# Performance work log

Hardware: AMD Instinct MI355X
Metric: run time of the kernel (lower is better)

The kernel has to match this reference:

```python
import jax, jax.numpy as jnp
import numpy as np

EPS = 1e-5

def rmsnorm(x, w):
    var = jnp.mean(x * x, axis=-1, keepdims=True)
    return x * jax.lax.rsqrt(var + EPS) * w

def apply_rope(x, cos, sin):
    # x: [B, S, H, D], cos/sin: [S, D//2]; llama-style complex rotation over pairs
    B, S, H, D = x.shape
    xr = x.reshape(B, S, H, D // 2, 2)
    x0, x1 = xr[..., 0], xr[..., 1]
    c = cos[None, :, None, :]
    s = sin[None, :, None, :]
    o0 = x0 * c - x1 * s
    o1 = x0 * s + x1 * c
    return jnp.stack([o0, o1], axis=-1).reshape(B, S, H, D)

def setup_inputs() -> dict:
    key = jax.random.key(0)
    ks = jax.random.split(key, 8)
    B, S, dim = 2, 2048, 2048
    H, nope, rope = 16, 128, 64
    q_lr, kv_lr = 1536, 512
    hd = nope + rope
    x = jax.random.normal(ks[0], (B, S, dim), jnp.float32)
    wd_q = jax.random.normal(ks[1], (dim, q_lr), jnp.float32) * (dim ** -0.5)
    wu_q = jax.random.normal(ks[2], (q_lr, H * hd), jnp.float32) * (q_lr ** -0.5)
    q_norm_w = jnp.ones((q_lr,), jnp.float32)
    wd_kv = jax.random.normal(ks[3], (dim, kv_lr + rope), jnp.float32) * (dim ** -0.5)
    wu_kv = jax.random.normal(ks[4], (kv_lr, H * 2 * nope), jnp.float32) * (kv_lr ** -0.5)
    kv_norm_w = jnp.ones((kv_lr,), jnp.float32)
    wo = jax.random.normal(ks[5], (H * nope, dim), jnp.float32) * ((H * nope) ** -0.5)
    pos = jnp.arange(S, dtype=jnp.float32)
    inv_freq = 1.0 / (10000.0 ** (jnp.arange(0, rope, 2, dtype=jnp.float32) / rope))
    ang = pos[:, None] * inv_freq[None, :]  # [S, rope//2]
    return {"x": x, "wd_q": wd_q, "wu_q": wu_q, "q_norm_w": q_norm_w,
            "wd_kv": wd_kv, "wu_kv": wu_kv, "kv_norm_w": kv_norm_w, "wo": wo,
            "cos": jnp.cos(ang), "sin": jnp.sin(ang), "start_pos": 0}

def reference(x, wd_q, wu_q, q_norm_w, wd_kv, wu_kv, kv_norm_w, wo, cos, sin, start_pos):
    B, S, dim = x.shape
    H, nope, rope = 16, 128, 64
    kv_lr = 512
    hd = nope + rope
    # low-rank Q projection + RMSNorm
    cq = x @ wd_q
    xq = rmsnorm(cq, q_norm_w) @ wu_q
    xq = xq.reshape(B, S, H, hd)
    xq_nope, xq_rope = xq[..., :nope], xq[..., nope:]
    # low-rank KV projection
    kvd = x @ wd_kv
    ckv, xk_rope = kvd[..., :kv_lr], kvd[..., kv_lr:]
    xk_rope = xk_rope.reshape(B, S, 1, rope)
    kvu = (rmsnorm(ckv, kv_norm_w) @ wu_kv).reshape(B, S, H, 2 * nope)
    xk_nope, xv = kvu[..., :nope], kvu[..., nope:]
    # partial RoPE
    xq_rope = apply_rope(xq_rope, cos, sin)
    xk_rope = apply_rope(xk_rope, cos, sin)
    xk_rope = jnp.broadcast_to(xk_rope, (B, S, H, rope))
    q = jnp.concatenate([xq_nope, xq_rope], axis=-1)  # [B,S,H,192]
    k = jnp.concatenate([xk_nope, xk_rope], axis=-1)
    # causal SDPA
    scale = 1.0 / jnp.sqrt(jnp.float32(hd))
    scores = jnp.einsum('bqhd,bkhd->bhqk', q, k) * scale
    mask = jnp.tril(jnp.ones((S, S), bool))
    scores = jnp.where(mask[None, None], scores, jnp.finfo(scores.dtype).min)
    attn = jax.nn.softmax(scores, axis=-1)
    out = jnp.einsum('bhqk,bkhd->bqhd', attn, xv).reshape(B, S, H * nope)
    return out @ wo
```

## Files before the change

### kernel.cpp

```cpp
#include <hip/hip_runtime.h>
#include <hip/hip_bf16.h>

#define S_LEN 2048
#define NHEAD 16
#define NOPE 128
#define ROPE 64
#define HD 192

typedef unsigned short ushort_t;
typedef __attribute__((ext_vector_type(8))) short short8;
typedef __attribute__((ext_vector_type(4))) float f32x4;

#define AS1 __attribute__((address_space(1)))
#define AS3 __attribute__((address_space(3)))

__device__ __forceinline__ unsigned short f2bf(float f) {
  unsigned int u = __float_as_uint(f);
  return (unsigned short)((u + 0x7FFFu + ((u >> 16) & 1u)) >> 16);
}

__global__ __launch_bounds__(256) void prep_k(const float* __restrict__ x, ushort_t* __restrict__ xb,
                                              const float* __restrict__ wd_q, ushort_t* __restrict__ wdqt,
                                              const float* __restrict__ wd_kv, ushort_t* __restrict__ wdkvt,
                                              const float* __restrict__ wu_q, ushort_t* __restrict__ wuqt,
                                              const float* __restrict__ wu_kv, ushort_t* __restrict__ wukvt,
                                              const float* __restrict__ wo, ushort_t* __restrict__ wot) {
  int id = blockIdx.x;
  if (id < 4096) {
    const int i = id * 256 + threadIdx.x;
    const float4 v0 = *(const float4*)&x[(size_t)i * 8];
    const float4 v1 = *(const float4*)&x[(size_t)i * 8 + 4];
    union { uint4 u; ushort_t s[8]; } pk;
    pk.s[0] = f2bf(v0.x); pk.s[1] = f2bf(v0.y); pk.s[2] = f2bf(v0.z); pk.s[3] = f2bf(v0.w);
    pk.s[4] = f2bf(v1.x); pk.s[5] = f2bf(v1.y); pk.s[6] = f2bf(v1.z); pk.s[7] = f2bf(v1.w);
    *(uint4*)&xb[(size_t)i * 8] = pk.u;
    return;
  }
  id -= 4096;
  const float* B; ushort_t* Bt; int K, N, gx;
  if (id < 3072)               { B = wd_q;  Bt = wdqt;  K = 2048; N = 1536; gx = 48;  }
  else if ((id -= 3072) < 1280){ B = wd_kv; Bt = wdkvt; K = 2048; N = 576;  gx = 20;  }
  else if ((id -= 1280) < 4608){ B = wu_q;  Bt = wuqt;  K = 1536; N = 3072; gx = 96;  }
  else if ((id -= 4608) < 2048){ B = wu_kv; Bt = wukvt; K = 512;  N = 4096; gx = 128; }
  else { id -= 2048;             B = wo;    Bt = wot;   K = 2048; N = 2048; gx = 64;  }
  __shared__ float tile[32][33];
  const int tx = threadIdx.x & 31, ty = threadIdx.x >> 5;
  const int n0 = (id % gx) * 32, k0 = (id / gx) * 32;
  if (n0 >= N) {
#pragma unroll
    for (int r = 0; r < 4; ++r)
      Bt[(size_t)(n0 + ty + 8 * r) * K + k0 + tx] = 0;
    return;
  }
#pragma unroll
  for (int r = 0; r < 4; ++r)
    tile[ty + 8 * r][tx] = B[(size_t)(k0 + ty + 8 * r) * N + n0 + tx];
  __syncthreads();
#pragma unroll
  for (int r = 0; r < 4; ++r)
    Bt[(size_t)(n0 + ty + 8 * r) * K + k0 + tx] = f2bf(tile[tx][ty + 8 * r]);
}

template<int EPI>
__global__ __launch_bounds__(512, 4) void mfma_gemm(const ushort_t* __restrict__ A,
                                                 const ushort_t* __restrict__ Bt,
                                                 float* __restrict__ C,
                                                 int M, int N, int K, int ldc,
                                                 ushort_t* __restrict__ kb16o,
                                                 ushort_t* __restrict__ vto,
                                                 float* __restrict__ C2,
                                                 const float* __restrict__ cosb,
                                                 const float* __restrict__ sinb) {
  __shared__ ushort_t As[2][128 * 32];
  __shared__ ushort_t Bs[2][128 * 32];
  const int tid = threadIdx.x;
  const int lane = tid & 63;
  const int wave = tid >> 6;
  const int wm = wave & 3, wn = wave >> 2;

  unsigned bxu = blockIdx.x, byu = blockIdx.y;
  {
    const unsigned gx = gridDim.x;
    const unsigned nwg = gx * gridDim.y;
    if ((nwg & 7u) == 0u) {
      unsigned flat = byu * gx + bxu;
      const unsigned cpx = nwg >> 3;
      flat = (flat & 7u) * cpx + (flat >> 3);
      bxu = flat % gx; byu = flat / gx;
    }
  }
  const int m0 = byu * 128, n0 = bxu * 128;
  const int l15 = lane & 15, quad = lane >> 4;

  f32x4 acc[2][4] = {};

  const int ma0 = tid >> 2;
  const int scol = (((tid & 3) ^ ((tid >> 3) & 3)) << 3);
  const int rsw = (l15 >> 1) & 3;

  typedef AS3 ushort_t lds_us;
  lds_us* AsL = (lds_us*)As;
  lds_us* BsL = (lds_us*)Bs;
  const int wbase = wave * 512;

  auto issue = [&](int k0, int buf) {
    __builtin_amdgcn_global_load_lds(
        (const AS1 void*)&A[(size_t)(m0 + ma0) * K + k0 + scol],
        (AS3 void*)(AsL + buf * 4096 + wbase), 16, 0, 0);
    __builtin_amdgcn_global_load_lds(
        (const AS1 void*)&Bt[(size_t)(n0 + ma0) * K + k0 + scol],
        (AS3 void*)(BsL + buf * 4096 + wbase), 16, 0, 0);
  };

  const int nk = K >> 5;
  issue(0, 0);
  __builtin_amdgcn_sched_barrier(0);

  for (int ks = 0; ks < nk; ++ks) {
    const int buf = ks & 1;
    const bool more = (ks + 1 < nk);
    if (more) {
      issue((ks + 1) << 5, buf ^ 1);
      __builtin_amdgcn_sched_barrier(0);
      asm volatile("s_waitcnt vmcnt(2)" ::: "memory");
    } else {
      asm volatile("s_waitcnt vmcnt(0)" ::: "memory");
    }
    __builtin_amdgcn_s_barrier();
    __builtin_amdgcn_sched_barrier(0);

    short8 af[2], bf[4];
#pragma unroll
    for (int i = 0; i < 2; ++i)
      af[i] = *(const short8*)&As[buf][(wm * 32 + i * 16 + l15) * 32 + ((quad ^ rsw) << 3)];
#pragma unroll
    for (int j = 0; j < 4; ++j)
      bf[j] = *(const short8*)&Bs[buf][(wn * 64 + j * 16 + l15) * 32 + ((quad ^ rsw) << 3)];
    __builtin_amdgcn_s_setprio(1);
#pragma unroll
    for (int i = 0; i < 2; ++i)
#pragma unroll
      for (int j = 0; j < 4; ++j)
        acc[i][j] = __builtin_amdgcn_mfma_f32_16x16x32_bf16(af[i], bf[j], acc[i][j], 0, 0, 0);
    __builtin_amdgcn_s_setprio(0);
    __builtin_amdgcn_s_barrier();
    __builtin_amdgcn_sched_barrier(0);
  }

  if constexpr (EPI == 0) {
#pragma unroll
    for (int i = 0; i < 2; ++i)
#pragma unroll
      for (int r = 0; r < 4; ++r) {
        const size_t rg = (size_t)(m0 + wm * 32 + i * 16 + quad * 4 + r);
#pragma unroll
        for (int j = 0; j < 4; ++j)
          C[rg * ldc + n0 + wn * 64 + j * 16 + l15] = acc[i][j][r];
      }
  } else if constexpr (EPI == 1) {
    const int h = n0 >> 8;
    const bool is_v = (n0 >> 7) & 1;
    if (!is_v) {
#pragma unroll
      for (int i = 0; i < 2; ++i)
#pragma unroll
        for (int r = 0; r < 4; ++r) {
          const size_t rg = (size_t)(m0 + wm * 32 + i * 16 + quad * 4 + r);
#pragma unroll
          for (int j = 0; j < 4; ++j)
            kb16o[rg * 2048 + h * 128 + wn * 64 + j * 16 + l15] = f2bf(acc[i][j][r]);
        }
    } else {
      __shared__ __align__(16) ushort_t trb[64 * 136];
      const int bb = m0 >> 11;
      const int m0loc = m0 & 2047;
      ushort_t* vbase = vto + ((size_t)(bb * NHEAD + h) * 128) * 2048;
#pragma unroll
      for (int vh = 0; vh < 2; ++vh) {
        if (wn == vh) {
#pragma unroll
          for (int i = 0; i < 2; ++i)
#pragma unroll
            for (int r = 0; r < 4; ++r) {
              const int tloc = wm * 32 + i * 16 + quad * 4 + r;
#pragma unroll
              for (int j = 0; j < 4; ++j)
                trb[(j * 16 + l15) * 136 + tloc] = f2bf(acc[i][j][r]);
            }
        }
        __syncthreads();
#pragma unroll
        for (int it = 0; it < 2; ++it) {
          const int u = tid + (it << 9);
          const int vdl = u >> 4, tc = u & 15;
          *(uint4*)&vbase[(size_t)(vh * 64 + vdl) * 2048 + m0loc + tc * 8] =
              *(const uint4*)&trb[vdl * 136 + tc * 8];
        }
        __syncthreads();
      }
    }
  } else if constexpr (EPI == 2) {
    float* Cd;
    int ldd, nc;
    if (n0 < 1536) { Cd = C;  ldd = 1536; nc = n0; }
    else           { Cd = C2; ldd = 640;  nc = n0 - 1536; }
#pragma unroll
    for (int i = 0; i < 2; ++i)
#pragma unroll
      for (int r = 0; r < 4; ++r) {
        const size_t rg = (size_t)(m0 + wm * 32 + i * 16 + quad * 4 + r);
#pragma unroll
        for (int j = 0; j < 4; ++j)
          Cd[rg * ldd + nc + wn * 64 + j * 16 + l15] = acc[i][j][r];
      }
  } else {
    const float qscale = 0.07216878364870323f;
#pragma unroll
    for (int i = 0; i < 2; ++i)
#pragma unroll
      for (int r = 0; r < 4; ++r) {
        const int rg = m0 + wm * 32 + i * 16 + quad * 4 + r;
        const int sp = rg & (S_LEN - 1);
#pragma unroll
        for (int j = 0; j < 4; ++j) {
          const int col = n0 + wn * 64 + j * 16 + l15;
          float val = acc[i][j][r] * qscale;
          const float pr = __shfl_xor(val, 1);
          const int dd = col % HD;
          float o = val;
          if (dd >= NOPE) {
            const int d = (dd - NOPE) >> 1;
            const float cc = cosb[sp * 32 + d];
            const float sn = sinb[sp * 32 + d];
            o = (lane & 1) ? (pr * sn + val * cc) : (val * cc - pr * sn);
          }
          kb16o[(size_t)rg * 3072 + col] = f2bf(o);
        }
      }
  }
}

__global__ __launch_bounds__(256) void rmsnorm2_k(const float* __restrict__ cq,
                                                  ushort_t* __restrict__ cqn,
                                                  const float* __restrict__ qw,
                                                  const float* __restrict__ kvd,
                                                  ushort_t* __restrict__ ckvn,
                                                  const float* __restrict__ kvw,
                                                  ushort_t* __restrict__ krope16,
                                                  const float* __restrict__ cosb,
                                                  const float* __restrict__ sinb) {
  const bool is_q = blockIdx.x < 4096;
  const int row = blockIdx.x & 4095;
  const int tid = threadIdx.x;
  const float* ip = is_q ? cq + (size_t)row * 1536 : kvd + (size_t)row * 640;
  ushort_t* op = is_q ? cqn + (size_t)row * 1536 : ckvn + (size_t)row * 512;
  const float* w = is_q ? qw : kvw;
  const int L = is_q ? 1536 : 512;
  const int nper = L >> 8;
  float r[6];
  float ss = 0.f;
  for (int j = 0; j < nper; ++j) {
    r[j] = ip[tid + (j << 8)];
    ss += r[j] * r[j];
  }
  for (int off = 32; off; off >>= 1) ss += __shfl_down(ss, off);
  __shared__ float wsum[4];
  __shared__ float scale_s;
  if ((tid & 63) == 0) wsum[tid >> 6] = ss;
  __syncthreads();
  if (tid == 0) {
    float t = wsum[0] + wsum[1] + wsum[2] + wsum[3];
    scale_s = rsqrtf(t / (float)L + 1e-5f);
  }
  __syncthreads();
  const float sc = scale_s;
  for (int j = 0; j < nper; ++j)
    op[tid + (j << 8)] = f2bf(r[j] * sc * w[tid + (j << 8)]);
  if (!is_q && tid < 32) {
    const int d = tid;
    const int s = row & (S_LEN - 1);
    const float c = cosb[s * 32 + d];
    const float sn = sinb[s * 32 + d];
    const float* kb = kvd + (size_t)row * 640 + 512;
    const float y0 = kb[2 * d], y1 = kb[2 * d + 1];
    union { unsigned int u; ushort_t s2[2]; } pk;
    pk.s2[0] = f2bf(y0 * c - y1 * sn);
    pk.s2[1] = f2bf(y0 * sn + y1 * c);
    *(unsigned int*)&krope16[(size_t)row * 64 + 2 * d] = pk.u;
  }
}

#define QT 128
#define KC 64
__global__ __launch_bounds__(1024, 4) void attn_k(const ushort_t* __restrict__ q16,
                                                  const ushort_t* __restrict__ kb16,
                                                  const ushort_t* __restrict__ vT,
                                                  const ushort_t* __restrict__ krope16,
                                                  ushort_t* __restrict__ outp) {
  const int bx = blockIdx.x;
  const int g = bx & 31;
  const int s = bx >> 5;
  const int tile = (s < 8) ? s : 23 - s;
  const int b = g >> 4, h = g & 15;
  const int q0 = tile * QT;
  const int tid = threadIdx.x;
  const int lane = tid & 63;
  const int wv = tid >> 6;
  const int wg = wv >> 3;
  const int wq8 = wv & 7;
  const int gtid = tid & 511;
  const int l15 = lane & 15, quad = lane >> 4;

  __shared__ __align__(16) ushort_t Kn[2][64 * 128];
  __shared__ __align__(16) ushort_t Kr[2][64 * 64];
  __shared__ __align__(16) ushort_t Vt[2][2][128 * 64];
  __shared__ __align__(16) ushort_t Pb[16][16 * 72];

  const int qbase = q0 + wq8 * 16;
  const size_t growq = (size_t)b * S_LEN + qbase;
  const ushort_t* vTh = vT + ((size_t)(b * NHEAD + h) * 128) * 2048;
  const size_t bbase = (size_t)b * S_LEN;

  typedef AS3 ushort_t lds_us;
  lds_us* KnL = (lds_us*)Kn;
  lds_us* KrL = (lds_us*)Kr;
  lds_us* VtL = (lds_us*)Vt;

  auto issueK = [&](int c) {
    const size_t growk = bbase + (size_t)c * KC;
#pragma unroll
    for (int it = 0; it < 2; ++it) {
      const int u = gtid + (it << 9);
      const int key = u >> 4, sl = u & 15;
      const int ss = sl ^ (key & 7);
      __builtin_amdgcn_global_load_lds(
          (const AS1 void*)&kb16[(growk + key) * 2048 + h * 128 + ss * 8],
          (AS3 void*)(KnL + wg * 8192 + it * 4096 + wq8 * 512), 16, 0, 0);
    }
    {
      const int u = gtid;
      const int key = u >> 3, sl = u & 7;
      const int ss = sl ^ (key & 7);
      __builtin_amdgcn_global_load_lds(
          (const AS1 void*)&krope16[(growk + key) * 64 + ss * 8],
          (AS3 void*)(KrL + wg * 4096 + wq8 * 512), 16, 0, 0);
    }
  };
  auto issueV = [&](int c, int buf) {
    const int j0 = c * KC;
#pragma unroll
    for (int it = 0; it < 2; ++it) {
      const int u = gtid + (it << 9);
      const int vd = u >> 3, sl = u & 7;
      const int ss = sl ^ (vd & 7);
      __builtin_amdgcn_global_load_lds(
          (const AS1 void*)&vTh[(size_t)vd * 2048 + j0 + ss * 8],
          (AS3 void*)(VtL + (wg * 2 + buf) * 8192 + it * 4096 + wq8 * 512), 16, 0, 0);
    }
  };

  const int nchunk = (q0 + QT) / KC;
  const int half = nchunk >> 1;
  const int cbase = wg * half;

  issueK(cbase);
  issueV(cbase, 0);
  __builtin_amdgcn_sched_barrier(0);

  short8 qf[6];
#pragma unroll
  for (int ks = 0; ks < 6; ++ks)
    qf[ks] = *(const short8*)&q16[(growq + l15) * 3072 + h * HD + ks * 32 + quad * 8];

  f32x4 oacc[8] = {};
  float mrow[4], lrow[4];
  int q_r[4];
#pragma unroll
  for (int r = 0; r < 4; ++r) {
    mrow[r] = -1e30f; lrow[r] = 0.f;
    q_r[r] = qbase + quad * 4 + r;
  }

  asm volatile("s_waitcnt vmcnt(2)" ::: "memory");
  __builtin_amdgcn_s_barrier();
  __builtin_amdgcn_sched_barrier(0);

  for (int cl = 0; cl < half; ++cl) {
    const int c = cbase + cl;
    const int j0 = c * KC;
    const bool more = (cl + 1 < half);
    const int buf = cl & 1;
    const bool skipw = (j0 > qbase + 15);

    f32x4 sacc[4] = {};
    if (!skipw) {
      __builtin_amdgcn_s_setprio(1);
#pragma unroll
      for (int ks = 0; ks < 6; ++ks) {
        short8 kf[4];
        if (ks < 4) {
#pragma unroll
          for (int kt = 0; kt < 4; ++kt)
            kf[kt] = *(const short8*)&Kn[wg][(kt * 16 + l15) * 128 + (((ks * 4 + quad) ^ (l15 & 7)) << 3)];
        } else {
#pragma unroll
          for (int kt = 0; kt < 4; ++kt)
            kf[kt] = *(const short8*)&Kr[wg][(kt * 16 + l15) * 64 + ((((ks - 4) * 4 + quad) ^ (l15 & 7)) << 3)];
        }
#pragma unroll
        for (int kt = 0; kt < 4; ++kt)
          sacc[kt] = __builtin_amdgcn_mfma_f32_16x16x32_bf16(qf[ks], kf[kt], sacc[kt], 0, 0, 0);
      }
      __builtin_amdgcn_s_setprio(0);
    }

    __builtin_amdgcn_s_barrier();
    if (more) issueK(c + 1);
    __builtin_amdgcn_sched_barrier(0);

    if (!skipw) {
      if (j0 + KC - 1 > qbase) {
#pragma unroll
        for (int kt = 0; kt < 4; ++kt) {
          const int key = j0 + kt * 16 + l15;
#pragma unroll
          for (int r = 0; r < 4; ++r)
            sacc[kt][r] = (key <= q_r[r]) ? sacc[kt][r] : -1e30f;
        }
      }
      float pmax[4];
#pragma unroll
      for (int r = 0; r < 4; ++r) {
        float mx = fmaxf(fmaxf(sacc[0][r], sacc[1][r]),
                         fmaxf(sacc[2][r], sacc[3][r]));
        mx = fmaxf(mx, __shfl_xor(mx, 1));
        mx = fmaxf(mx, __shfl_xor(mx, 2));
        mx = fmaxf(mx, __shfl_xor(mx, 4));
        mx = fmaxf(mx, __shfl_xor(mx, 8));
        pmax[r] = mx;
      }
      bool need = false;
#pragma unroll
      for (int r = 0; r < 4; ++r)
        need = need || (pmax[r] > mrow[r] + 8.0f);
      const bool upd = __any(need);
      float alpha[4];
      if (upd) {
#pragma unroll
        for (int r = 0; r < 4; ++r) {
          const float mn = fmaxf(mrow[r], pmax[r]);
          alpha[r] = __expf(mrow[r] - mn);
          mrow[r] = mn;
        }
      }
#pragma unroll
      for (int kt = 0; kt < 4; ++kt)
#pragma unroll
        for (int r = 0; r < 4; ++r)
          sacc[kt][r] = __expf(sacc[kt][r] - mrow[r]);
#pragma unroll
      for (int r = 0; r < 4; ++r) {
        float rs = sacc[0][r] + sacc[1][r] + sacc[2][r] + sacc[3][r];
        rs += __shfl_xor(rs, 1);
        rs += __shfl_xor(rs, 2);
        rs += __shfl_xor(rs, 4);
        rs += __shfl_xor(rs, 8);
        lrow[r] = upd ? lrow[r] * alpha[r] + rs : lrow[r] + rs;
      }
#pragma unroll
      for (int kt = 0; kt < 4; ++kt)
#pragma unroll
        for (int r = 0; r < 4; ++r)
          Pb[wv][(quad * 4 + r) * 72 + kt * 16 + l15] = f2bf(sacc[kt][r]);
      if (upd) {
#pragma unroll
        for (int nt = 0; nt < 8; ++nt)
#pragma unroll
          for (int r = 0; r < 4; ++r)
            oacc[nt][r] *= alpha[r];
      }
    }

    if (more) asm volatile("s_waitcnt vmcnt(3)" ::: "memory");
    else      asm volatile("s_waitcnt vmcnt(0)" ::: "memory");
    __builtin_amdgcn_s_barrier();
    __builtin_amdgcn_sched_barrier(0);

    if (!skipw) {
      __builtin_amdgcn_s_setprio(1);
#pragma unroll
      for (int st = 0; st < 2; ++st) {
        const short8 pf = *(const short8*)&Pb[wv][l15 * 72 + st * 32 + quad * 8];
#pragma unroll
        for (int nt = 0; nt < 8; ++nt) {
          const short8 vf = *(const short8*)&Vt[wg][buf][(nt * 16 + l15) * 64 + (((st * 4 + quad) ^ (l15 & 7)) << 3)];
          oacc[nt] = __builtin_amdgcn_mfma_f32_16x16x32_bf16(pf, vf, oacc[nt], 0, 0, 0);
        }
      }
      __builtin_amdgcn_s_setprio(0);
    }

    if (more) {
      issueV(c + 1, buf ^ 1);
      __builtin_amdgcn_sched_barrier(0);
      asm volatile("s_waitcnt vmcnt(2)" ::: "memory");
      __builtin_amdgcn_s_barrier();
      __builtin_amdgcn_sched_barrier(0);
    }
  }

  __builtin_amdgcn_s_barrier();
  float* Ocmb = (float*)&Vt[0][0][0];
  float* Mlb  = (float*)&Kn[0][0];
  if (wg == 1) {
#pragma unroll
    for (int nt = 0; nt < 8; ++nt)
#pragma unroll
      for (int r = 0; r < 4; ++r)
        Ocmb[(size_t)(wq8 * 16 + quad * 4 + r) * 128 + nt * 16 + l15] = oacc[nt][r];
    if (l15 == 0) {
#pragma unroll
      for (int r = 0; r < 4; ++r) {
        Mlb[(wq8 * 16 + quad * 4 + r) * 2 + 0] = mrow[r];
        Mlb[(wq8 * 16 + quad * 4 + r) * 2 + 1] = lrow[r];
      }
    }
  }
  __builtin_amdgcn_s_barrier();
  if (wg == 0) {
#pragma unroll
    for (int r = 0; r < 4; ++r) {
      const int row = wq8 * 16 + quad * 4 + r;
      const float m1 = Mlb[row * 2 + 0];
      const float l1 = Mlb[row * 2 + 1];
      const float mx = fmaxf(mrow[r], m1);
      const float w0 = __expf(mrow[r] - mx);
      const float w1 = __expf(m1 - mx);
      const float inv = 1.0f / (lrow[r] * w0 + l1 * w1);
      const size_t orow = growq + quad * 4 + r;
#pragma unroll
      for (int nt = 0; nt < 8; ++nt) {
        const float o = oacc[nt][r] * w0 + Ocmb[(size_t)row * 128 + nt * 16 + l15] * w1;
        outp[orow * 2048 + h * 128 + nt * 16 + l15] = f2bf(o * inv);
      }
    }
  }
}

extern "C" void kernel_launch(void* const* d_in, const int* in_sizes, int n_in,
                              void* d_out, int out_size, void* d_ws, size_t ws_size,
                              hipStream_t stream) {
  const float* x        = (const float*)d_in[0];
  const float* wd_q     = (const float*)d_in[1];
  const float* wu_q     = (const float*)d_in[2];
  const float* q_norm_w = (const float*)d_in[3];
  const float* wd_kv    = (const float*)d_in[4];
  const float* wu_kv    = (const float*)d_in[5];
  const float* kv_norm_w= (const float*)d_in[6];
  const float* wo       = (const float*)d_in[7];
  const float* cosb     = (const float*)d_in[8];
  const float* sinb     = (const float*)d_in[9];
  float* out = (float*)d_out;

  char* ws = (char*)d_ws;
  float*    cq    = (float*)(ws + 0);
  ushort_t* q16   = (ushort_t*)(ws + 0);
  ushort_t* kb16  = (ushort_t*)(ws + 50331648);
  ushort_t* vT    = (ushort_t*)(ws + 67108864);
  ushort_t* xb    = (ushort_t*)(ws + 83886080);
  ushort_t* cqn   = (ushort_t*)(ws + 117440512);
  float*    kvd   = (float*)(ws + 130023424);
  ushort_t* ckvn  = (ushort_t*)(ws + 140509184);
  ushort_t* aoutb = (ushort_t*)(ws + 130023424);
  ushort_t* krope16 = (ushort_t*)(ws + 146800640);
  ushort_t* wdqt  = (ushort_t*)(ws + 147849216);
  ushort_t* wdkvt = (ushort_t*)(ws + 154140672);
  ushort_t* wuqt  = (ushort_t*)(ws + 156762112);
  ushort_t* wukvt = (ushort_t*)(ws + 166199296);
  ushort_t* wot   = (ushort_t*)(ws + 170393600);

  const int M = 2 * S_LEN;
  dim3 blk(256);
  dim3 blk512(512);

  prep_k<<<19200, blk, 0, stream>>>(x, xb, wd_q, wdqt, wd_kv, wdkvt,
                                    wu_q, wuqt, wu_kv, wukvt, wo, wot);

  mfma_gemm<2><<<dim3(2176 / 128, M / 128), blk512, 0, stream>>>(
      xb, wdqt, cq, M, 2176, 2048, 1536, nullptr, nullptr, kvd, nullptr, nullptr);
  rmsnorm2_k<<<2 * M, 256, 0, stream>>>(cq, cqn, q_norm_w, kvd, ckvn, kv_norm_w,
                                        krope16, cosb, sinb);
  mfma_gemm<3><<<dim3(3072 / 128, M / 128), blk512, 0, stream>>>(
      cqn, wuqt, nullptr, M, 3072, 1536, 0, q16, nullptr, nullptr, cosb, sinb);
  mfma_gemm<1><<<dim3(4096 / 128, M / 128), blk512, 0, stream>>>(
      ckvn, wukvt, nullptr, M, 4096, 512, 0, kb16, vT, nullptr, nullptr, nullptr);
  attn_k<<<2 * NHEAD * (S_LEN / QT), 1024, 0, stream>>>(q16, kb16, vT, krope16, aoutb);
  mfma_gemm<0><<<dim3(2048 / 128, M / 128), blk512, 0, stream>>>(
      aoutb, wot, out, M, 2048, 2048, 2048, nullptr, nullptr, nullptr, nullptr, nullptr);
}
```

Baseline: 444.5 us.

## Merge Q and KV up-projection GEMMs into one launch with triple-buffered loads

```diff
diff --git a/kernel.cpp b/kernel.cpp
--- a/kernel.cpp
+++ b/kernel.cpp
@@ -70,16 +70,32 @@
                                                  ushort_t* __restrict__ vto,
                                                  float* __restrict__ C2,
                                                  const float* __restrict__ cosb,
-                                                 const float* __restrict__ sinb) {
-  __shared__ ushort_t As[2][128 * 32];
-  __shared__ ushort_t Bs[2][128 * 32];
+                                                 const float* __restrict__ sinb,
+                                                 const ushort_t* __restrict__ A2,
+                                                 const ushort_t* __restrict__ Bt2,
+                                                 ushort_t* __restrict__ kb2) {
+  __shared__ __align__(16) ushort_t As[3][128 * 32];
+  __shared__ __align__(16) ushort_t Bs[3][128 * 32];
   const int tid = threadIdx.x;
   const int lane = tid & 63;
   const int wave = tid >> 6;
   const int wm = wave & 3, wn = wave >> 2;
 
-  unsigned bxu = blockIdx.x, byu = blockIdx.y;
-  {
+  const ushort_t* Ax;
+  const ushort_t* Btx;
+  int Kx;
+  bool isq = true;
+  int m0, n0;
+  if constexpr (EPI == 4) {
+    int flat = blockIdx.x;
+    flat = (flat & 7) * 224 + (flat >> 3);
+    isq = flat < 768;
+    int bxl, byl;
+    if (isq) { bxl = flat % 24;  byl = flat / 24;  Ax = A;  Btx = Bt;  Kx = 1536; }
+    else     { int f = flat - 768; bxl = f % 32; byl = f / 32; Ax = A2; Btx = Bt2; Kx = 512; }
+    m0 = byl * 128; n0 = bxl * 128;
+  } else {
+    unsigned bxu = blockIdx.x, byu = blockIdx.y;
     const unsigned gx = gridDim.x;
     const unsigned nwg = gx * gridDim.y;
     if ((nwg & 7u) == 0u) {
@@ -88,8 +104,9 @@
       flat = (flat & 7u) * cpx + (flat >> 3);
       bxu = flat % gx; byu = flat / gx;
     }
-  }
-  const int m0 = byu * 128, n0 = bxu * 128;
+    m0 = byu * 128; n0 = bxu * 128;
+    Ax = A; Btx = Bt; Kx = K;
+  }
   const int l15 = lane & 15, quad = lane >> 4;
 
   f32x4 acc[2][4] = {};
@@ -105,23 +122,26 @@
 
   auto issue = [&](int k0, int buf) {
     __builtin_amdgcn_global_load_lds(
-        (const AS1 void*)&A[(size_t)(m0 + ma0) * K + k0 + scol],
+        (const AS1 void*)&Ax[(size_t)(m0 + ma0) * Kx + k0 + scol],
         (AS3 void*)(AsL + buf * 4096 + wbase), 16, 0, 0);
     __builtin_amdgcn_global_load_lds(
-        (const AS1 void*)&Bt[(size_t)(n0 + ma0) * K + k0 + scol],
+        (const AS1 void*)&Btx[(size_t)(n0 + ma0) * Kx + k0 + scol],
         (AS3 void*)(BsL + buf * 4096 + wbase), 16, 0, 0);
   };
 
-  const int nk = K >> 5;
+  const int nk = Kx >> 5;
   issue(0, 0);
+  issue(32, 1);
   __builtin_amdgcn_sched_barrier(0);
 
+  int buf = 0;
   for (int ks = 0; ks < nk; ++ks) {
-    const int buf = ks & 1;
-    const bool more = (ks + 1 < nk);
-    if (more) {
-      issue((ks + 1) << 5, buf ^ 1);
+    if (ks + 2 < nk) {
+      int b2 = buf + 2; if (b2 >= 3) b2 -= 3;
+      issue((ks + 2) << 5, b2);
       __builtin_amdgcn_sched_barrier(0);
+      asm volatile("s_waitcnt vmcnt(4)" ::: "memory");
+    } else if (ks + 1 < nk) {
       asm volatile("s_waitcnt vmcnt(2)" ::: "memory");
     } else {
       asm volatile("s_waitcnt vmcnt(0)" ::: "memory");
@@ -145,6 +165,7 @@
     __builtin_amdgcn_s_setprio(0);
     __builtin_amdgcn_s_barrier();
     __builtin_amdgcn_sched_barrier(0);
+    ++buf; if (buf == 3) buf = 0;
   }
 
   if constexpr (EPI == 0) {
@@ -157,48 +178,6 @@
         for (int j = 0; j < 4; ++j)
           C[rg * ldc + n0 + wn * 64 + j * 16 + l15] = acc[i][j][r];
       }
-  } else if constexpr (EPI == 1) {
-    const int h = n0 >> 8;
-    const bool is_v = (n0 >> 7) & 1;
-    if (!is_v) {
-#pragma unroll
-      for (int i = 0; i < 2; ++i)
-#pragma unroll
-        for (int r = 0; r < 4; ++r) {
-          const size_t rg = (size_t)(m0 + wm * 32 + i * 16 + quad * 4 + r);
-#pragma unroll
-          for (int j = 0; j < 4; ++j)
-            kb16o[rg * 2048 + h * 128 + wn * 64 + j * 16 + l15] = f2bf(acc[i][j][r]);
-        }
-    } else {
-      __shared__ __align__(16) ushort_t trb[64 * 136];
-      const int bb = m0 >> 11;
-      const int m0loc = m0 & 2047;
-      ushort_t* vbase = vto + ((size_t)(bb * NHEAD + h) * 128) * 2048;
-#pragma unroll
-      for (int vh = 0; vh < 2; ++vh) {
-        if (wn == vh) {
-#pragma unroll
-          for (int i = 0; i < 2; ++i)
-#pragma unroll
-            for (int r = 0; r < 4; ++r) {
-              const int tloc = wm * 32 + i * 16 + quad * 4 + r;
-#pragma unroll
-              for (int j = 0; j < 4; ++j)
-                trb[(j * 16 + l15) * 136 + tloc] = f2bf(acc[i][j][r]);
-            }
-        }
-        __syncthreads();
-#pragma unroll
-        for (int it = 0; it < 2; ++it) {
-          const int u = tid + (it << 9);
-          const int vdl = u >> 4, tc = u & 15;
-          *(uint4*)&vbase[(size_t)(vh * 64 + vdl) * 2048 + m0loc + tc * 8] =
-              *(const uint4*)&trb[vdl * 136 + tc * 8];
-        }
-        __syncthreads();
-      }
-    }
   } else if constexpr (EPI == 2) {
     float* Cd;
     int ldd, nc;
@@ -213,30 +192,74 @@
         for (int j = 0; j < 4; ++j)
           Cd[rg * ldd + nc + wn * 64 + j * 16 + l15] = acc[i][j][r];
       }
-  } else {
-    const float qscale = 0.07216878364870323f;
-#pragma unroll
-    for (int i = 0; i < 2; ++i)
-#pragma unroll
-      for (int r = 0; r < 4; ++r) {
-        const int rg = m0 + wm * 32 + i * 16 + quad * 4 + r;
-        const int sp = rg & (S_LEN - 1);
-#pragma unroll
-        for (int j = 0; j < 4; ++j) {
-          const int col = n0 + wn * 64 + j * 16 + l15;
-          float val = acc[i][j][r] * qscale;
-          const float pr = __shfl_xor(val, 1);
-          const int dd = col % HD;
-          float o = val;
-          if (dd >= NOPE) {
-            const int d = (dd - NOPE) >> 1;
-            const float cc = cosb[sp * 32 + d];
-            const float sn = sinb[sp * 32 + d];
-            o = (lane & 1) ? (pr * sn + val * cc) : (val * cc - pr * sn);
+  } else if constexpr (EPI == 4) {
+    if (isq) {
+      const float qscale = 0.07216878364870323f;
+#pragma unroll
+      for (int i = 0; i < 2; ++i)
+#pragma unroll
+        for (int r = 0; r < 4; ++r) {
+          const int rg = m0 + wm * 32 + i * 16 + quad * 4 + r;
+          const int sp = rg & (S_LEN - 1);
+#pragma unroll
+          for (int j = 0; j < 4; ++j) {
+            const int col = n0 + wn * 64 + j * 16 + l15;
+            float val = acc[i][j][r] * qscale;
+            const float pr = __shfl_xor(val, 1);
+            const int dd = col % HD;
+            float o = val;
+            if (dd >= NOPE) {
+              const int d = (dd - NOPE) >> 1;
+              const float cc = cosb[sp * 32 + d];
+              const float sn = sinb[sp * 32 + d];
+              o = (lane & 1) ? (pr * sn + val * cc) : (val * cc - pr * sn);
+            }
+            kb16o[(size_t)rg * 3072 + col] = f2bf(o);
           }
-          kb16o[(size_t)rg * 3072 + col] = f2bf(o);
         }
-      }
+    } else {
+      const int h = n0 >> 8;
+      const bool is_v = (n0 >> 7) & 1;
+      if (!is_v) {
+#pragma unroll
+        for (int i = 0; i < 2; ++i)
+#pragma unroll
+          for (int r = 0; r < 4; ++r) {
+            const size_t rg = (size_t)(m0 + wm * 32 + i * 16 + quad * 4 + r);
+#pragma unroll
+            for (int j = 0; j < 4; ++j)
+              kb2[rg * 2048 + h * 128 + wn * 64 + j * 16 + l15] = f2bf(acc[i][j][r]);
+          }
+      } else {
+        ushort_t* trb = (ushort_t*)&As[0][0];
+        const int bb = m0 >> 11;
+        const int m0loc = m0 & 2047;
+        ushort_t* vbase = vto + ((size_t)(bb * NHEAD + h) * 128) * 2048;
+#pragma unroll
+        for (int vh = 0; vh < 2; ++vh) {
+          if (wn == vh) {
+#pragma unroll
+            for (int i = 0; i < 2; ++i)
+#pragma unroll
+              for (int r = 0; r < 4; ++r) {
+                const int tloc = wm * 32 + i * 16 + quad * 4 + r;
+#pragma unroll
+                for (int j = 0; j < 4; ++j)
+                  trb[(j * 16 + l15) * 136 + tloc] = f2bf(acc[i][j][r]);
+              }
+          }
+          __syncthreads();
+#pragma unroll
+          for (int it = 0; it < 2; ++it) {
+            const int u = tid + (it << 9);
+            const int vdl = u >> 4, tc = u & 15;
+            *(uint4*)&vbase[(size_t)(vh * 64 + vdl) * 2048 + m0loc + tc * 8] =
+                *(const uint4*)&trb[vdl * 136 + tc * 8];
+          }
+          __syncthreads();
+        }
+      }
+    }
   }
 }
 
@@ -587,14 +610,15 @@
                                     wu_q, wuqt, wu_kv, wukvt, wo, wot);
 
   mfma_gemm<2><<<dim3(2176 / 128, M / 128), blk512, 0, stream>>>(
-      xb, wdqt, cq, M, 2176, 2048, 1536, nullptr, nullptr, kvd, nullptr, nullptr);
+      xb, wdqt, cq, M, 2176, 2048, 1536, nullptr, nullptr, kvd, nullptr, nullptr,
+      nullptr, nullptr, nullptr);
   rmsnorm2_k<<<2 * M, 256, 0, stream>>>(cq, cqn, q_norm_w, kvd, ckvn, kv_norm_w,
                                         krope16, cosb, sinb);
-  mfma_gemm<3><<<dim3(3072 / 128, M / 128), blk512, 0, stream>>>(
-      cqn, wuqt, nullptr, M, 3072, 1536, 0, q16, nullptr, nullptr, cosb, sinb);
-  mfma_gemm<1><<<dim3(4096 / 128, M / 128), blk512, 0, stream>>>(
-      ckvn, wukvt, nullptr, M, 4096, 512, 0, kb16, vT, nullptr, nullptr, nullptr);
+  mfma_gemm<4><<<dim3(1792), blk512, 0, stream>>>(
+      cqn, wuqt, nullptr, M, 0, 0, 0, q16, vT, nullptr, cosb, sinb,
+      ckvn, wukvt, kb16);
   attn_k<<<2 * NHEAD * (S_LEN / QT), 1024, 0, stream>>>(q16, kb16, vT, krope16, aoutb);
   mfma_gemm<0><<<dim3(2048 / 128, M / 128), blk512, 0, stream>>>(
-      aoutb, wot, out, M, 2048, 2048, 2048, nullptr, nullptr, nullptr, nullptr, nullptr);
+      aoutb, wot, out, M, 2048, 2048, 2048, nullptr, nullptr, nullptr, nullptr, nullptr,
+      nullptr, nullptr, nullptr);
 }
```

After: 481.0 us. 8.2% more time.
